# Kernel tuning notes

Measured on AMD Instinct MI355X. Metric: run time of the kernel, lower is better.

Reference implementation:

```python
import math
import jax, jax.numpy as jnp
import numpy as np

INPUT_DIM = 1024


def setup_inputs() -> dict:
    key = jax.random.key(0)
    k1, k2, k3 = jax.random.split(key, 3)
    x = jax.random.normal(k1, (16, INPUT_DIM, 64, 64), dtype=jnp.float32)
    # Conv2d(input_dim, 1, kernel_size=1): weight [1, C, 1, 1] -> store as [C], bias [1]
    fan_in = INPUT_DIM
    bound = 1.0 / math.sqrt(fan_in)
    key_w = jax.random.uniform(k2, (INPUT_DIM,), minval=-bound, maxval=bound, dtype=jnp.float32)
    key_b = jax.random.uniform(k3, (1,), minval=-bound, maxval=bound, dtype=jnp.float32)
    return {"x": x, "key_w": key_w, "key_b": key_b}


def reference(x, key_w, key_b):
    B, C, H, W = x.shape
    scale = 1.0 / math.sqrt(C)
    # 1x1 conv C->1 == channel contraction; logits over spatial positions
    logits = (jnp.einsum('bchw,c->bhw', x, key_w) + key_b[0]) * scale  # [B,H,W]
    attn = jax.nn.softmax(logits.reshape(B, H * W).astype(jnp.float32), axis=-1)  # [B,HW]
    rs_x = x.reshape(B, C, H * W)
    focus = jnp.einsum('bcs,bs->bc', rs_x, attn)  # weighted channel sum
    return focus.reshape(B, C, 1, 1)
```

## Files before the change

kernel.cpp:

```cpp
#include <hip/hip_runtime.h>
#include <math.h>

#define BB 16
#define CC 1024
#define SS 4096
#define CCHUNKS 8
#define CPER (CC / CCHUNKS)
#define SCHUNKS 4
#define SPER (SS / SCHUNKS)

__global__ __launch_bounds__(256) void k_partial_logits(
    const float* __restrict__ x, const float* __restrict__ w,
    float* __restrict__ partial)
{
    const int schunk = blockIdx.x;
    const int cchunk = blockIdx.y;
    const int b      = blockIdx.z;
    const int tid    = threadIdx.x;
    const int s      = schunk * SPER + tid * 4;

    const float* xb = x + (size_t)b * CC * SS;
    const int c0 = cchunk * CPER;

    float4 acc = make_float4(0.f, 0.f, 0.f, 0.f);
    for (int i = 0; i < CPER; ++i) {
        const int c = c0 + i;
        const float wc = w[c];
        const float4 xv = *(const float4*)(xb + (size_t)c * SS + s);
        acc.x += xv.x * wc;
        acc.y += xv.y * wc;
        acc.z += xv.z * wc;
        acc.w += xv.w * wc;
    }
    *(float4*)(partial + ((size_t)(b * CCHUNKS + cchunk) * SS + s)) = acc;
}

__global__ __launch_bounds__(1024) void k_softmax(
    const float* __restrict__ partial, const float* __restrict__ bias,
    float* __restrict__ attn)
{
    const int b   = blockIdx.x;
    const int tid = threadIdx.x;
    const int s   = tid * 4;
    const int wave = tid >> 6;
    const int lane = tid & 63;

    float4 l = make_float4(0.f, 0.f, 0.f, 0.f);
    for (int k = 0; k < CCHUNKS; ++k) {
        const float4 p =
            *(const float4*)(partial + ((size_t)(b * CCHUNKS + k) * SS + s));
        l.x += p.x; l.y += p.y; l.z += p.z; l.w += p.w;
    }
    const float scale = 0.03125f;
    const float bv = bias[0];
    l.x = (l.x + bv) * scale;
    l.y = (l.y + bv) * scale;
    l.z = (l.z + bv) * scale;
    l.w = (l.w + bv) * scale;

    float m = fmaxf(fmaxf(l.x, l.y), fmaxf(l.z, l.w));
    for (int off = 32; off; off >>= 1) m = fmaxf(m, __shfl_down(m, off));
    __shared__ float redm[16];
    __shared__ float reds[16];
    if (lane == 0) redm[wave] = m;
    __syncthreads();
    if (wave == 0) {
        float v = (lane < 16) ? redm[lane] : -INFINITY;
        for (int off = 8; off; off >>= 1) v = fmaxf(v, __shfl_down(v, off));
        if (lane == 0) redm[0] = v;
    }
    __syncthreads();
    const float M = redm[0];

    float4 e;
    e.x = __expf(l.x - M);
    e.y = __expf(l.y - M);
    e.z = __expf(l.z - M);
    e.w = __expf(l.w - M);

    float ssum = (e.x + e.y) + (e.z + e.w);
    for (int off = 32; off; off >>= 1) ssum += __shfl_down(ssum, off);
    if (lane == 0) reds[wave] = ssum;
    __syncthreads();
    if (wave == 0) {
        float v = (lane < 16) ? reds[lane] : 0.f;
        for (int off = 8; off; off >>= 1) v += __shfl_down(v, off);
        if (lane == 0) reds[0] = v;
    }
    __syncthreads();
    const float inv = 1.0f / reds[0];

    float4 a = make_float4(e.x * inv, e.y * inv, e.z * inv, e.w * inv);
    *(float4*)(attn + (size_t)b * SS + s) = a;
}

__global__ __launch_bounds__(256) void k_focus(
    const float* __restrict__ x, const float* __restrict__ attn,
    float* __restrict__ out)
{
    __shared__ float a_lds[SS];
    const int b    = blockIdx.y;
    const int c    = blockIdx.x * 4 + (threadIdx.x >> 6);
    const int lane = threadIdx.x & 63;

    for (int i = 0; i < 4; ++i) {
        const int idx = i * 1024 + threadIdx.x * 4;
        *(float4*)(a_lds + idx) = *(const float4*)(attn + (size_t)b * SS + idx);
    }
    __syncthreads();

    const float* xr = x + ((size_t)(b * CC + c) * SS);
    float4 acc = make_float4(0.f, 0.f, 0.f, 0.f);
    for (int j = 0; j < 16; ++j) {
        const int s = j * 256 + lane * 4;
        const float4 xv = *(const float4*)(xr + s);
        const float4 av = *(const float4*)(a_lds + s);
        acc.x += xv.x * av.x;
        acc.y += xv.y * av.y;
        acc.z += xv.z * av.z;
        acc.w += xv.w * av.w;
    }
    float v = (acc.x + acc.y) + (acc.z + acc.w);
    for (int off = 32; off; off >>= 1) v += __shfl_down(v, off);
    if (lane == 0) out[b * CC + c] = v;
}

extern "C" void kernel_launch(void* const* d_in, const int* in_sizes, int n_in,
                              void* d_out, int out_size, void* d_ws, size_t ws_size,
                              hipStream_t stream) {
    const float* x    = (const float*)d_in[0];
    const float* w    = (const float*)d_in[1];
    const float* bias = (const float*)d_in[2];
    float* out = (float*)d_out;

    float* partial = (float*)d_ws;
    float* attn    = partial + (size_t)BB * CCHUNKS * SS;

    k_partial_logits<<<dim3(SCHUNKS, CCHUNKS, BB), 256, 0, stream>>>(x, w, partial);
    k_softmax<<<BB, 1024, 0, stream>>>(partial, bias, attn);
    k_focus<<<dim3(CC / 4, BB), 256, 0, stream>>>(x, attn, out);
}
```

Before: 399.3 us.

## Fuse logits, softmax and weighted sum into single-pass online-softmax kernel

Replaces the three-kernel pipeline (partial logits, softmax, focus) with one fused kernel that reads each x tile once. It computes logits, updates a running max and sum in flash-attention style, and accumulates rescaled weighted channel sums per spatial block. A small combine kernel then merges the per-block partials using the block maxima and sums. This halves the HBM traffic on x, which was previously read twice. The cost is per-chunk block-wide syncs and LDS reductions, plus fewer loads in flight per thread.

```diff
diff --git a/kernel.cpp b/kernel.cpp
--- a/kernel.cpp
+++ b/kernel.cpp
@@ -4,125 +4,162 @@
 #define BB 16
 #define CC 1024
 #define SS 4096
-#define CCHUNKS 8
-#define CPER (CC / CCHUNKS)
-#define SCHUNKS 4
-#define SPER (SS / SCHUNKS)
+#define SCH 16
+#define NCH 4
+#define SPB (SCH * NCH)
+#define KBLK (SS / SPB)
 
-__global__ __launch_bounds__(256) void k_partial_logits(
+__global__ __launch_bounds__(512, 4) void k_fused(
     const float* __restrict__ x, const float* __restrict__ w,
-    float* __restrict__ partial)
+    const float* __restrict__ bias,
+    float* __restrict__ Nk, float* __restrict__ mk, float* __restrict__ sk)
 {
-    const int schunk = blockIdx.x;
-    const int cchunk = blockIdx.y;
-    const int b      = blockIdx.z;
-    const int tid    = threadIdx.x;
-    const int s      = schunk * SPER + tid * 4;
+    __shared__ float4 red4[512];
+    __shared__ float4 out1[128];
+    __shared__ float4 l16f4[4];
+    __shared__ float4 e4_lds[4];
+    __shared__ float  alpha_lds;
+
+    const int kblk = blockIdx.x;
+    const int b    = blockIdx.y;
+    const int t    = threadIdx.x;
+    const int q    = t >> 2;
+    const int m    = t & 3;
 
     const float* xb = x + (size_t)b * CC * SS;
-    const int c0 = cchunk * CPER;
 
-    float4 acc = make_float4(0.f, 0.f, 0.f, 0.f);
-    for (int i = 0; i < CPER; ++i) {
-        const int c = c0 + i;
-        const float wc = w[c];
-        const float4 xv = *(const float4*)(xb + (size_t)c * SS + s);
-        acc.x += xv.x * wc;
-        acc.y += xv.y * wc;
-        acc.z += xv.z * wc;
-        acc.w += xv.w * wc;
+    float wreg[8];
+#pragma unroll
+    for (int i = 0; i < 8; ++i) wreg[i] = w[q + 128 * i];
+
+    float bv = 0.f;
+    if (t < 16) bv = bias[0];
+
+    float4 np[8];
+#pragma unroll
+    for (int i = 0; i < 8; ++i) np[i] = make_float4(0.f, 0.f, 0.f, 0.f);
+    float m_run = -1e30f, s_run = 0.f;
+
+#pragma unroll 1
+    for (int ch = 0; ch < NCH; ++ch) {
+        const int s0 = kblk * SPB + ch * SCH + m * 4;
+
+        float4 xv[8];
+#pragma unroll
+        for (int i = 0; i < 8; ++i)
+            xv[i] = *(const float4*)(xb + (size_t)(q + 128 * i) * SS + s0);
+
+        float4 lacc = make_float4(0.f, 0.f, 0.f, 0.f);
+#pragma unroll
+        for (int i = 0; i < 8; ++i) {
+            lacc.x += xv[i].x * wreg[i];
+            lacc.y += xv[i].y * wreg[i];
+            lacc.z += xv[i].z * wreg[i];
+            lacc.w += xv[i].w * wreg[i];
+        }
+        red4[m * 128 + q] = lacc;
+        __syncthreads();
+
+        if (t < 128) {
+            const int mm = t >> 5, ii = t & 31;
+            float4 v = red4[mm * 128 + ii];
+            float4 a2 = red4[mm * 128 + ii + 32];
+            float4 a3 = red4[mm * 128 + ii + 64];
+            float4 a4 = red4[mm * 128 + ii + 96];
+            v.x += a2.x + a3.x + a4.x;
+            v.y += a2.y + a3.y + a4.y;
+            v.z += a2.z + a3.z + a4.z;
+            v.w += a2.w + a3.w + a4.w;
+            out1[mm * 32 + ii] = v;
+        }
+        __syncthreads();
+
+        if (t < 32) {
+            const int mm = t >> 3, ii = t & 7;
+            float4 v = out1[mm * 32 + ii];
+            float4 a2 = out1[mm * 32 + ii + 8];
+            float4 a3 = out1[mm * 32 + ii + 16];
+            float4 a4 = out1[mm * 32 + ii + 24];
+            v.x += a2.x + a3.x + a4.x;
+            v.y += a2.y + a3.y + a4.y;
+            v.z += a2.z + a3.z + a4.z;
+            v.w += a2.w + a3.w + a4.w;
+            for (int d = 4; d; d >>= 1) {
+                v.x += __shfl_down(v.x, d);
+                v.y += __shfl_down(v.y, d);
+                v.z += __shfl_down(v.z, d);
+                v.w += __shfl_down(v.w, d);
+            }
+            if (ii == 0) l16f4[mm] = v;
+        }
+        __syncthreads();
+
+        if (t < 16) {
+            float l = (((const float*)l16f4)[t] + bv) * 0.03125f;
+            float mc = l;
+            for (int d = 8; d; d >>= 1) mc = fmaxf(mc, __shfl_xor(mc, d));
+            const float mnew = fmaxf(m_run, mc);
+            const float a = __expf(m_run - mnew);
+            const float e = __expf(l - mnew);
+            float cs = e;
+            for (int d = 8; d; d >>= 1) cs += __shfl_xor(cs, d);
+            s_run = s_run * a + cs;
+            m_run = mnew;
+            ((float*)e4_lds)[t] = e;
+            if (t == 0) alpha_lds = a;
+        }
+        __syncthreads();
+
+        const float a = alpha_lds;
+        const float4 e4 = e4_lds[m];
+#pragma unroll
+        for (int i = 0; i < 8; ++i) {
+            np[i].x = np[i].x * a + xv[i].x * e4.x;
+            np[i].y = np[i].y * a + xv[i].y * e4.y;
+            np[i].z = np[i].z * a + xv[i].z * e4.z;
+            np[i].w = np[i].w * a + xv[i].w * e4.w;
+        }
     }
-    *(float4*)(partial + ((size_t)(b * CCHUNKS + cchunk) * SS + s)) = acc;
+
+#pragma unroll
+    for (int i = 0; i < 8; ++i) {
+        float v = (np[i].x + np[i].y) + (np[i].z + np[i].w);
+        v += __shfl_down(v, 1);
+        v += __shfl_down(v, 2);
+        if (m == 0)
+            Nk[((size_t)(b * KBLK + kblk)) * CC + q + 128 * i] = v;
+    }
+    if (t == 0) {
+        mk[b * KBLK + kblk] = m_run;
+        sk[b * KBLK + kblk] = s_run;
+    }
 }
 
-__global__ __launch_bounds__(1024) void k_softmax(
-    const float* __restrict__ partial, const float* __restrict__ bias,
-    float* __restrict__ attn)
+__global__ __launch_bounds__(64) void k_combine(
+    const float* __restrict__ Nk, const float* __restrict__ mk,
+    const float* __restrict__ sk, float* __restrict__ out)
 {
-    const int b   = blockIdx.x;
-    const int tid = threadIdx.x;
-    const int s   = tid * 4;
-    const int wave = tid >> 6;
-    const int lane = tid & 63;
+    __shared__ float ek[KBLK];
+    const int b  = blockIdx.y;
+    const int c0 = blockIdx.x * 64;
+    const int t  = threadIdx.x;
 
-    float4 l = make_float4(0.f, 0.f, 0.f, 0.f);
-    for (int k = 0; k < CCHUNKS; ++k) {
-        const float4 p =
-            *(const float4*)(partial + ((size_t)(b * CCHUNKS + k) * SS + s));
-        l.x += p.x; l.y += p.y; l.z += p.z; l.w += p.w;
-    }
-    const float scale = 0.03125f;
-    const float bv = bias[0];
-    l.x = (l.x + bv) * scale;
-    l.y = (l.y + bv) * scale;
-    l.z = (l.z + bv) * scale;
-    l.w = (l.w + bv) * scale;
-
-    float m = fmaxf(fmaxf(l.x, l.y), fmaxf(l.z, l.w));
-    for (int off = 32; off; off >>= 1) m = fmaxf(m, __shfl_down(m, off));
-    __shared__ float redm[16];
-    __shared__ float reds[16];
-    if (lane == 0) redm[wave] = m;
-    __syncthreads();
-    if (wave == 0) {
-        float v = (lane < 16) ? redm[lane] : -INFINITY;
-        for (int off = 8; off; off >>= 1) v = fmaxf(v, __shfl_down(v, off));
-        if (lane == 0) redm[0] = v;
-    }
-    __syncthreads();
-    const float M = redm[0];
-
-    float4 e;
-    e.x = __expf(l.x - M);
-    e.y = __expf(l.y - M);
-    e.z = __expf(l.z - M);
-    e.w = __expf(l.w - M);
-
-    float ssum = (e.x + e.y) + (e.z + e.w);
-    for (int off = 32; off; off >>= 1) ssum += __shfl_down(ssum, off);
-    if (lane == 0) reds[wave] = ssum;
-    __syncthreads();
-    if (wave == 0) {
-        float v = (lane < 16) ? reds[lane] : 0.f;
-        for (int off = 8; off; off >>= 1) v += __shfl_down(v, off);
-        if (lane == 0) reds[0] = v;
-    }
-    __syncthreads();
-    const float inv = 1.0f / reds[0];
-
-    float4 a = make_float4(e.x * inv, e.y * inv, e.z * inv, e.w * inv);
-    *(float4*)(attn + (size_t)b * SS + s) = a;
-}
-
-__global__ __launch_bounds__(256) void k_focus(
-    const float* __restrict__ x, const float* __restrict__ attn,
-    float* __restrict__ out)
-{
-    __shared__ float a_lds[SS];
-    const int b    = blockIdx.y;
-    const int c    = blockIdx.x * 4 + (threadIdx.x >> 6);
-    const int lane = threadIdx.x & 63;
-
-    for (int i = 0; i < 4; ++i) {
-        const int idx = i * 1024 + threadIdx.x * 4;
-        *(float4*)(a_lds + idx) = *(const float4*)(attn + (size_t)b * SS + idx);
-    }
+    const float mv = mk[b * KBLK + t];
+    const float sv = sk[b * KBLK + t];
+    float M = mv;
+    for (int d = 32; d; d >>= 1) M = fmaxf(M, __shfl_xor(M, d));
+    const float e = __expf(mv - M);
+    float D = sv * e;
+    for (int d = 32; d; d >>= 1) D += __shfl_xor(D, d);
+    ek[t] = e / D;
     __syncthreads();
 
-    const float* xr = x + ((size_t)(b * CC + c) * SS);
-    float4 acc = make_float4(0.f, 0.f, 0.f, 0.f);
-    for (int j = 0; j < 16; ++j) {
-        const int s = j * 256 + lane * 4;
-        const float4 xv = *(const float4*)(xr + s);
-        const float4 av = *(const float4*)(a_lds + s);
-        acc.x += xv.x * av.x;
-        acc.y += xv.y * av.y;
-        acc.z += xv.z * av.z;
-        acc.w += xv.w * av.w;
-    }
-    float v = (acc.x + acc.y) + (acc.z + acc.w);
-    for (int off = 32; off; off >>= 1) v += __shfl_down(v, off);
-    if (lane == 0) out[b * CC + c] = v;
+    float acc = 0.f;
+    const float* Nb = Nk + (size_t)b * KBLK * CC + c0 + t;
+#pragma unroll 4
+    for (int k = 0; k < KBLK; ++k)
+        acc += Nb[(size_t)k * CC] * ek[k];
+    out[b * CC + c0 + t] = acc;
 }
 
 extern "C" void kernel_launch(void* const* d_in, const int* in_sizes, int n_in,
@@ -133,10 +170,10 @@
     const float* bias = (const float*)d_in[2];
     float* out = (float*)d_out;
 
-    float* partial = (float*)d_ws;
-    float* attn    = partial + (size_t)BB * CCHUNKS * SS;
+    float* Nk = (float*)d_ws;
+    float* mk = Nk + (size_t)BB * KBLK * CC;
+    float* sk = mk + BB * KBLK;
 
-    k_partial_logits<<<dim3(SCHUNKS, CCHUNKS, BB), 256, 0, stream>>>(x, w, partial);
-    k_softmax<<<BB, 1024, 0, stream>>>(partial, bias, attn);
-    k_focus<<<dim3(CC / 4, BB), 256, 0, stream>>>(x, attn, out);
+    k_fused<<<dim3(KBLK, BB), 512, 0, stream>>>(x, w, bias, Nk, mk, sk);
+    k_combine<<<dim3(CC / 64, BB), 64, 0, stream>>>(Nk, mk, sk, out);
 }
```

Result: faster. 386.6 us (-3.2%).
